# Optimization experiments

Measured on AMD Instinct MI355X. Metric: run time of the kernel, lower is better.

The kernel has to match this reference:

```python
import jax, jax.numpy as jnp
import numpy as np

N_HEADS = 18
HEAD_DIM = 16
ROPE_THETA = 10000.0
SLIDING_WINDOW = 4096


def _rotate_half(x):
    half = x.shape[-1] // 2
    return jnp.concatenate([-x[..., half:], x[..., :half]], axis=-1)


def setup_inputs() -> dict:
    key = jax.random.key(0)
    k0, k1, k2, k3, k4 = jax.random.split(key, 5)
    B, S, H = 2, 2048, 288
    std = 0.02
    return {
        "hidden_states": jax.random.normal(k0, (B, S, H), dtype=jnp.float32),
        "Wq": jax.random.normal(k1, (H, H), dtype=jnp.float32) * std,
        "Wk": jax.random.normal(k2, (H, H), dtype=jnp.float32) * std,
        "Wv": jax.random.normal(k3, (H, H), dtype=jnp.float32) * std,
        "Wo": jax.random.normal(k4, (H, H), dtype=jnp.float32) * std,
    }


def reference(hidden_states, Wq, Wk, Wv, Wo):
    B, S, H = hidden_states.shape
    nH, D = N_HEADS, HEAD_DIM

    # QKV projections (nn.Linear: y = x @ W.T), reshape to [B, nH, S, D]
    def proj(W):
        return jnp.einsum("bsh,oh->bso", hidden_states, W).reshape(B, S, nH, D).transpose(0, 2, 1, 3)

    q, k, v = proj(Wq), proj(Wk), proj(Wv)

    # Rotary embedding: position_ids = arange(S)
    pos = jnp.arange(S, dtype=jnp.float32)
    inv_freq = 1.0 / (ROPE_THETA ** (jnp.arange(0, D, 2, dtype=jnp.float32) / D))
    freqs = pos[:, None] * inv_freq[None, :]            # [S, D/2]
    emb = jnp.concatenate([freqs, freqs], axis=-1)      # [S, D]
    cos = jnp.cos(emb)[None, None, :, :]                # [1, 1, S, D]
    sin = jnp.sin(emb)[None, None, :, :]
    q = q * cos + _rotate_half(q) * sin
    k = k * cos + _rotate_half(k) * sin

    # num_key_value_groups = 1 -> repeat_kv is identity.
    scores = jnp.einsum("bhqd,bhkd->bhqk", q, k) / jnp.sqrt(jnp.float32(D))

    # Sliding-window causal mask: attend iff 0 <= i - j < window
    i = jnp.arange(S)[:, None]
    j = jnp.arange(S)[None, :]
    allowed = (j <= i) & (i - j < SLIDING_WINDOW)       # [S, S]
    neg = jnp.finfo(scores.dtype).min
    scores = jnp.where(allowed[None, None, :, :], scores, neg)

    attn = jax.nn.softmax(scores.astype(jnp.float32), axis=-1).astype(q.dtype)
    out = jnp.einsum("bhqk,bhkd->bhqd", attn, v)        # [B, nH, S, D]
    out = out.transpose(0, 2, 1, 3).reshape(B, S, H)
    return jnp.einsum("bsh,oh->bso", out, Wo)
```

## Files before the change

kernel.cpp:

```cpp
#include <hip/hip_runtime.h>
#include <hip/hip_bf16.h>
#include <math.h>

#define H_DIM 288
#define NHEADS 18
#define HEAD_D 16
#define SEQ 2048
#define BATCH 2
#define M_TOT (BATCH*SEQ)
#define XCNT (M_TOT*H_DIM)
#define WCNT (H_DIM*H_DIM)
#define NUNITS 10368
#define NQUNITS 2304

typedef _Float16 f16_t;
typedef __attribute__((ext_vector_type(2))) _Float16 half2v;
typedef __attribute__((ext_vector_type(4))) _Float16 half4v;
typedef __attribute__((ext_vector_type(8))) _Float16 half8v;
typedef __attribute__((ext_vector_type(4))) float   float4v;

__global__ __launch_bounds__(256) void cvt_f16(
    const float* __restrict__ X,
    const float* __restrict__ Wq, const float* __restrict__ Wk,
    const float* __restrict__ Wv, const float* __restrict__ Wo,
    f16_t* __restrict__ Xf, f16_t* __restrict__ Wf)
{
    int idx = blockIdx.x * 256 + threadIdx.x;
    const int X4 = XCNT/4, W4 = WCNT/4;
    if (idx >= X4 + 4*W4) return;
    const float* src; f16_t* dst; int off;
    if (idx < X4) { src = X; dst = Xf; off = idx; }
    else {
        int r = idx - X4;
        int wz = r / W4; off = r - wz*W4;
        src = (wz==0) ? Wq : (wz==1) ? Wk : (wz==2) ? Wv : Wo;
        dst = Wf + (size_t)wz*WCNT;
    }
    float4 v = ((const float4*)src)[off];
    half4v h; h[0]=(f16_t)v.x; h[1]=(f16_t)v.y; h[2]=(f16_t)v.z; h[3]=(f16_t)v.w;
    ((half4v*)dst)[off] = h;
}

__global__ __launch_bounds__(64) void qkv_mfma(
    const f16_t* __restrict__ Xf, const f16_t* __restrict__ Wf,
    f16_t* __restrict__ Q16, f16_t* __restrict__ K16, f16_t* __restrict__ Vt)
{
    const int bx = blockIdx.x;
    const int z  = bx/6;
    const int n0 = (bx - z*6)*48;
    const int m0 = blockIdx.y*32;
    const int lane = threadIdx.x & 63;
    const int n = lane & 15, quad = lane >> 4;

    const f16_t* W = Wf + (size_t)z*WCNT;

    float4v acc[2][3];
    #pragma unroll
    for (int mt = 0; mt < 2; mt++)
        #pragma unroll
        for (int nt = 0; nt < 3; nt++)
            acc[mt][nt] = (float4v){0.f,0.f,0.f,0.f};

    for (int k0 = 0; k0 < H_DIM; k0 += 32) {
        half8v a[2], b[3];
        #pragma unroll
        for (int mt = 0; mt < 2; mt++)
            a[mt] = *(const half8v*)(Xf + (size_t)(m0 + mt*16 + n)*H_DIM + k0 + quad*8);
        #pragma unroll
        for (int nt = 0; nt < 3; nt++)
            b[nt] = *(const half8v*)(W + (size_t)(n0 + nt*16 + n)*H_DIM + k0 + quad*8);
        #pragma unroll
        for (int mt = 0; mt < 2; mt++)
            #pragma unroll
            for (int nt = 0; nt < 3; nt++)
                acc[mt][nt] = __builtin_amdgcn_mfma_f32_16x16x32_f16(a[mt], b[nt], acc[mt][nt], 0, 0, 0);
    }

    if (z < 2) {
        f16_t* dst = (z == 0) ? Q16 : K16;
        const float invf_rev = exp2f(-1.6609640474436813f * (float)(n & 7))
                             * 0.15915494309189535f;
        #pragma unroll
        for (int mt = 0; mt < 2; mt++) {
            #pragma unroll
            for (int r = 0; r < 4; r++) {
                int m = m0 + mt*16 + quad*4 + r;
                int bb = m >> 11, s = m & (SEQ - 1);
                float rev = (float)s * invf_rev;
                float fr = rev - floorf(rev);
                float sn = __builtin_amdgcn_sinf(fr);
                float c  = __builtin_amdgcn_cosf(fr);
                #pragma unroll
                for (int nt = 0; nt < 3; nt++) {
                    float own = acc[mt][nt][r];
                    float par = __shfl_xor(own, 8, 64);
                    float val = (n & 8) ? fmaf(own, c, par*sn) : fmaf(own, c, -par*sn);
                    if (z == 0) val *= 0.36067376022224085f;
                    int head = (n0 >> 4) + nt;
                    dst[((size_t)((bb*NHEADS + head)*SEQ) + s)*HEAD_D + n] = (f16_t)val;
                }
            }
        }
    } else {
        #pragma unroll
        for (int mt = 0; mt < 2; mt++)
            #pragma unroll
            for (int nt = 0; nt < 3; nt++)
                #pragma unroll
                for (int r = 0; r < 4; r++) {
                    int m = m0 + mt*16 + quad*4 + r;
                    int bb = m >> 11, s = m & (SEQ - 1);
                    int head = (n0 >> 4) + nt;
                    Vt[(size_t)(bb*NHEADS + head)*(SEQ*HEAD_D)
                       + (size_t)(s >> 4)*256 + n*16 + (s & 15)] = (f16_t)acc[mt][nt][r];
                }
    }
}

__device__ __forceinline__ half4v pack4(const float p[4]) {
    half2v ab = __builtin_bit_cast(half2v, __builtin_amdgcn_cvt_pkrtz(p[0], p[1]));
    half2v cd = __builtin_bit_cast(half2v, __builtin_amdgcn_cvt_pkrtz(p[2], p[3]));
    half4v o; o[0]=ab[0]; o[1]=ab[1]; o[2]=cd[0]; o[3]=cd[1];
    return o;
}

__global__ __launch_bounds__(256) void attn_part(
    const f16_t* __restrict__ Q16, const f16_t* __restrict__ K16,
    const f16_t* __restrict__ Vt,
    float4* __restrict__ accbuf, float* __restrict__ lbuf)
{
    const int bid = blockIdx.x;
    const int swz = (bid & 7) * 324 + (bid >> 3);
    const int unit = swz*4 + (threadIdx.x >> 6);
    const int lane = threadIdx.x & 63;
    const int n = lane & 15, quad = lane >> 4;

    const int bh = unit / 288;
    const int rem = unit - bh*288;
    int g, t0;
    if      (rem < 8)   { g=0; t0=rem;     }
    else if (rem < 24)  { g=1; t0=rem-8;   }
    else if (rem < 48)  { g=2; t0=rem-24;  }
    else if (rem < 80)  { g=3; t0=rem-48;  }
    else if (rem < 120) { g=4; t0=rem-80;  }
    else if (rem < 168) { g=5; t0=rem-120; }
    else if (rem < 224) { g=6; t0=rem-168; }
    else                { g=7; t0=rem-224; }
    const int qd = t0 / (g+1);
    const int qp = 8*g + qd;
    const int chunk = t0 - qd*(g+1);
    const int q0 = qp*32;

    half4v qb0 = *(const half4v*)(Q16 + ((size_t)bh*SEQ + q0 + n)*HEAD_D + quad*4);
    half4v qb1 = *(const half4v*)(Q16 + ((size_t)bh*SEQ + q0 + 16 + n)*HEAD_D + quad*4);
    const f16_t* Kb = K16 + (size_t)bh * SEQ * HEAD_D;
    const f16_t* Vb = Vt  + (size_t)bh * SEQ * HEAD_D;
    const int loff = n*16 + quad*4;

    const float4v zero = {0.f, 0.f, 0.f, 0.f};
    float4v acc0 = zero, acc1 = zero;
    float l0 = 0.f, l1 = 0.f;

    const int lim0 = 2*qp, lim1 = 2*qp + 1;
    const int ktlo = chunk*16;
    const int kthi = min(ktlo + 15, lim1);

    if (ktlo + 15 < lim0) {
        half4v KA[16], VA[16];
        #pragma unroll
        for (int i = 0; i < 16; i++) {
            KA[i] = *(const half4v*)(Kb + (size_t)(ktlo + i)*256 + loff);
            VA[i] = *(const half4v*)(Vb + (size_t)(ktlo + i)*256 + loff);
        }
        __builtin_amdgcn_s_setprio(1);
        #pragma unroll
        for (int i = 0; i < 16; i++) {
            float4v s1 = __builtin_amdgcn_mfma_f32_16x16x16f16(KA[i], qb1, zero, 0, 0, 0);
            float4v s0 = __builtin_amdgcn_mfma_f32_16x16x16f16(KA[i], qb0, zero, 0, 0, 0);
            float p1[4], p0[4];
            #pragma unroll
            for (int r = 0; r < 4; r++) { p1[r] = __builtin_amdgcn_exp2f(s1[r]); p0[r] = __builtin_amdgcn_exp2f(s0[r]); }
            l1 += (p1[0]+p1[1]) + (p1[2]+p1[3]);
            l0 += (p0[0]+p0[1]) + (p0[2]+p0[3]);
            acc1 = __builtin_amdgcn_mfma_f32_16x16x16f16(VA[i], pack4(p1), acc1, 0, 0, 0);
            acc0 = __builtin_amdgcn_mfma_f32_16x16x16f16(VA[i], pack4(p0), acc0, 0, 0, 0);
        }
        __builtin_amdgcn_s_setprio(0);
    } else {
        int kt = ktlo;
        half4v ka = *(const half4v*)(Kb + (size_t)kt*256 + loff);
        half4v va = *(const half4v*)(Vb + (size_t)kt*256 + loff);
        for (; kt <= kthi; kt++) {
            half4v kan, van;
            if (kt < kthi) {
                kan = *(const half4v*)(Kb + (size_t)(kt+1)*256 + loff);
                van = *(const half4v*)(Vb + (size_t)(kt+1)*256 + loff);
            }
            {
                float4v s = __builtin_amdgcn_mfma_f32_16x16x16f16(ka, qb1, zero, 0, 0, 0);
                float p[4];
                #pragma unroll
                for (int r = 0; r < 4; r++) {
                    float e = __builtin_amdgcn_exp2f(s[r]);
                    p[r] = (kt == lim1 && quad*4 + r > n) ? 0.0f : e;
                }
                l1 += (p[0]+p[1]) + (p[2]+p[3]);
                acc1 = __builtin_amdgcn_mfma_f32_16x16x16f16(va, pack4(p), acc1, 0, 0, 0);
            }
            if (kt <= lim0) {
                float4v s = __builtin_amdgcn_mfma_f32_16x16x16f16(ka, qb0, zero, 0, 0, 0);
                float p[4];
                #pragma unroll
                for (int r = 0; r < 4; r++) {
                    float e = __builtin_amdgcn_exp2f(s[r]);
                    p[r] = (kt == lim0 && quad*4 + r > n) ? 0.0f : e;
                }
                l0 += (p[0]+p[1]) + (p[2]+p[3]);
                acc0 = __builtin_amdgcn_mfma_f32_16x16x16f16(va, pack4(p), acc0, 0, 0, 0);
            }
            ka = kan; va = van;
        }
    }

    float4 a0; a0.x=acc0[0]; a0.y=acc0[1]; a0.z=acc0[2]; a0.w=acc0[3];
    float4 a1; a1.x=acc1[0]; a1.y=acc1[1]; a1.z=acc1[2]; a1.w=acc1[3];
    accbuf[((size_t)unit*2 + 0)*64 + lane] = a0;
    accbuf[((size_t)unit*2 + 1)*64 + lane] = a1;
    lbuf[((size_t)unit*2 + 0)*64 + lane] = l0;
    lbuf[((size_t)unit*2 + 1)*64 + lane] = l1;
}

__global__ __launch_bounds__(256) void attn_red(
    const float4* __restrict__ accbuf, const float* __restrict__ lbuf,
    f16_t* __restrict__ Of)
{
    const int bid = blockIdx.x;
    const int swz = (bid & 7) * 72 + (bid >> 3);
    const int wid = swz*4 + (threadIdx.x >> 6);
    const int lane = threadIdx.x & 63;
    const int n = lane & 15, quad = lane >> 4;
    const int bh = wid >> 6, qp = wid & 63;
    const int b = bh / NHEADS, h = bh - b*NHEADS;
    const int g = qp >> 3, j = qp & 7;
    const int nch = g + 1;
    const int ubase = bh*288 + qp + 4*g*(g-1) + g*j;

    #pragma unroll
    for (int t = 0; t < 2; t++) {
        float4 a = {0.f, 0.f, 0.f, 0.f};
        float l = 0.f;
        #pragma unroll
        for (int c = 0; c < 8; c++) {
            const int  cc = (c < nch) ? c : (nch - 1);
            const float m = (c < nch) ? 1.0f : 0.0f;
            size_t idx = ((size_t)(ubase + cc)*2 + t)*64 + lane;
            float4 v = accbuf[idx];
            float lv = lbuf[idx];
            a.x = fmaf(v.x, m, a.x); a.y = fmaf(v.y, m, a.y);
            a.z = fmaf(v.z, m, a.z); a.w = fmaf(v.w, m, a.w);
            l   = fmaf(lv,  m, l);
        }
        l += __shfl_xor(l, 16, 64);
        l += __shfl_xor(l, 32, 64);
        float inv = 1.0f / l;
        half4v o;
        o[0]=(f16_t)(a.x*inv); o[1]=(f16_t)(a.y*inv);
        o[2]=(f16_t)(a.z*inv); o[3]=(f16_t)(a.w*inv);
        *(half4v*)(Of + (size_t)(b*SEQ + qp*32 + t*16 + n)*H_DIM + h*HEAD_D + quad*4) = o;
    }
}

__global__ __launch_bounds__(64) void out_mfma(
    const f16_t* __restrict__ Of, const f16_t* __restrict__ Wo16,
    float* __restrict__ C)
{
    const int n0 = blockIdx.x * 48;
    const int m0 = blockIdx.y * 32;
    const int lane = threadIdx.x & 63;
    const int n = lane & 15, quad = lane >> 4;

    float4v acc[2][3];
    #pragma unroll
    for (int mt = 0; mt < 2; mt++)
        #pragma unroll
        for (int nt = 0; nt < 3; nt++)
            acc[mt][nt] = (float4v){0.f,0.f,0.f,0.f};

    for (int k0 = 0; k0 < H_DIM; k0 += 32) {
        half8v a[2], b[3];
        #pragma unroll
        for (int mt = 0; mt < 2; mt++)
            a[mt] = *(const half8v*)(Of + (size_t)(m0 + mt*16 + n)*H_DIM + k0 + quad*8);
        #pragma unroll
        for (int nt = 0; nt < 3; nt++)
            b[nt] = *(const half8v*)(Wo16 + (size_t)(n0 + nt*16 + n)*H_DIM + k0 + quad*8);
        #pragma unroll
        for (int mt = 0; mt < 2; mt++)
            #pragma unroll
            for (int nt = 0; nt < 3; nt++)
                acc[mt][nt] = __builtin_amdgcn_mfma_f32_16x16x32_f16(a[mt], b[nt], acc[mt][nt], 0, 0, 0);
    }
    #pragma unroll
    for (int mt = 0; mt < 2; mt++)
        #pragma unroll
        for (int nt = 0; nt < 3; nt++)
            #pragma unroll
            for (int r = 0; r < 4; r++) {
                int m = m0 + mt*16 + quad*4 + r;
                C[(size_t)m*H_DIM + n0 + nt*16 + n] = acc[mt][nt][r];
            }
}

extern "C" void kernel_launch(void* const* d_in, const int* in_sizes, int n_in,
                              void* d_out, int out_size, void* d_ws, size_t ws_size,
                              hipStream_t stream)
{
    const float* Xh = (const float*)d_in[0];
    const float* Wq = (const float*)d_in[1];
    const float* Wk = (const float*)d_in[2];
    const float* Wv = (const float*)d_in[3];
    const float* Wo = (const float*)d_in[4];
    float* out = (float*)d_out;

    f16_t* Xf  = (f16_t*)d_ws;
    f16_t* Wf  = Xf + XCNT;
    f16_t* Q16 = Wf + 4*(size_t)WCNT;
    f16_t* K16 = Q16 + XCNT;
    f16_t* Vt  = K16 + XCNT;
    f16_t* Of  = Vt + XCNT;
    float4* accbuf = (float4*)(Of + XCNT);
    float*  lbuf   = (float*)(accbuf + (size_t)NUNITS*2*64);

    const int total4 = (XCNT + 4*WCNT)/4;
    cvt_f16<<<dim3((total4 + 255)/256), 256, 0, stream>>>(Xh, Wq, Wk, Wv, Wo, Xf, Wf);
    qkv_mfma<<<dim3(18, 128), 64, 0, stream>>>(Xf, Wf, Q16, K16, Vt);
    attn_part<<<dim3(NUNITS/4), 256, 0, stream>>>(Q16, K16, Vt, accbuf, lbuf);
    attn_red<<<dim3(NQUNITS/4), 256, 0, stream>>>(accbuf, lbuf, Of);
    out_mfma<<<dim3(6, 128), 64, 0, stream>>>(Of, Wf + 3*(size_t)WCNT, out);
}
```

Measured before the change: 113.7 us.

## Split attention and QKV work into smaller per-wave tiles for more parallelism

After: 119.6 us. +5.2%, slower.

```diff
diff --git a/kernel.cpp b/kernel.cpp
--- a/kernel.cpp
+++ b/kernel.cpp
@@ -11,6 +11,7 @@
 #define XCNT (M_TOT*H_DIM)
 #define WCNT (H_DIM*H_DIM)
 #define NUNITS 10368
+#define NUU    20736
 #define NQUNITS 2304
 
 typedef _Float16 f16_t;
@@ -48,32 +49,26 @@
     const int bx = blockIdx.x;
     const int z  = bx/6;
     const int n0 = (bx - z*6)*48;
-    const int m0 = blockIdx.y*32;
+    const int m0 = blockIdx.y*16;
     const int lane = threadIdx.x & 63;
     const int n = lane & 15, quad = lane >> 4;
 
     const f16_t* W = Wf + (size_t)z*WCNT;
 
-    float4v acc[2][3];
+    float4v acc[3];
     #pragma unroll
-    for (int mt = 0; mt < 2; mt++)
-        #pragma unroll
-        for (int nt = 0; nt < 3; nt++)
-            acc[mt][nt] = (float4v){0.f,0.f,0.f,0.f};
+    for (int nt = 0; nt < 3; nt++)
+        acc[nt] = (float4v){0.f,0.f,0.f,0.f};
 
     for (int k0 = 0; k0 < H_DIM; k0 += 32) {
-        half8v a[2], b[3];
-        #pragma unroll
-        for (int mt = 0; mt < 2; mt++)
-            a[mt] = *(const half8v*)(Xf + (size_t)(m0 + mt*16 + n)*H_DIM + k0 + quad*8);
+        half8v a = *(const half8v*)(Xf + (size_t)(m0 + n)*H_DIM + k0 + quad*8);
+        half8v b[3];
         #pragma unroll
         for (int nt = 0; nt < 3; nt++)
             b[nt] = *(const half8v*)(W + (size_t)(n0 + nt*16 + n)*H_DIM + k0 + quad*8);
         #pragma unroll
-        for (int mt = 0; mt < 2; mt++)
-            #pragma unroll
-            for (int nt = 0; nt < 3; nt++)
-                acc[mt][nt] = __builtin_amdgcn_mfma_f32_16x16x32_f16(a[mt], b[nt], acc[mt][nt], 0, 0, 0);
+        for (int nt = 0; nt < 3; nt++)
+            acc[nt] = __builtin_amdgcn_mfma_f32_16x16x32_f16(a, b[nt], acc[nt], 0, 0, 0);
     }
 
     if (z < 2) {
@@ -81,39 +76,34 @@
         const float invf_rev = exp2f(-1.6609640474436813f * (float)(n & 7))
                              * 0.15915494309189535f;
         #pragma unroll
-        for (int mt = 0; mt < 2; mt++) {
-            #pragma unroll
-            for (int r = 0; r < 4; r++) {
-                int m = m0 + mt*16 + quad*4 + r;
-                int bb = m >> 11, s = m & (SEQ - 1);
-                float rev = (float)s * invf_rev;
-                float fr = rev - floorf(rev);
-                float sn = __builtin_amdgcn_sinf(fr);
-                float c  = __builtin_amdgcn_cosf(fr);
-                #pragma unroll
-                for (int nt = 0; nt < 3; nt++) {
-                    float own = acc[mt][nt][r];
-                    float par = __shfl_xor(own, 8, 64);
-                    float val = (n & 8) ? fmaf(own, c, par*sn) : fmaf(own, c, -par*sn);
-                    if (z == 0) val *= 0.36067376022224085f;
-                    int head = (n0 >> 4) + nt;
-                    dst[((size_t)((bb*NHEADS + head)*SEQ) + s)*HEAD_D + n] = (f16_t)val;
-                }
+        for (int r = 0; r < 4; r++) {
+            int m = m0 + quad*4 + r;
+            int bb = m >> 11, s = m & (SEQ - 1);
+            float rev = (float)s * invf_rev;
+            float fr = rev - floorf(rev);
+            float sn = __builtin_amdgcn_sinf(fr);
+            float c  = __builtin_amdgcn_cosf(fr);
+            #pragma unroll
+            for (int nt = 0; nt < 3; nt++) {
+                float own = acc[nt][r];
+                float par = __shfl_xor(own, 8, 64);
+                float val = (n & 8) ? fmaf(own, c, par*sn) : fmaf(own, c, -par*sn);
+                if (z == 0) val *= 0.36067376022224085f;
+                int head = (n0 >> 4) + nt;
+                dst[((size_t)((bb*NHEADS + head)*SEQ) + s)*HEAD_D + n] = (f16_t)val;
             }
         }
     } else {
         #pragma unroll
-        for (int mt = 0; mt < 2; mt++)
-            #pragma unroll
-            for (int nt = 0; nt < 3; nt++)
-                #pragma unroll
-                for (int r = 0; r < 4; r++) {
-                    int m = m0 + mt*16 + quad*4 + r;
-                    int bb = m >> 11, s = m & (SEQ - 1);
-                    int head = (n0 >> 4) + nt;
-                    Vt[(size_t)(bb*NHEADS + head)*(SEQ*HEAD_D)
-                       + (size_t)(s >> 4)*256 + n*16 + (s & 15)] = (f16_t)acc[mt][nt][r];
-                }
+        for (int nt = 0; nt < 3; nt++)
+            #pragma unroll
+            for (int r = 0; r < 4; r++) {
+                int m = m0 + quad*4 + r;
+                int bb = m >> 11, s = m & (SEQ - 1);
+                int head = (n0 >> 4) + nt;
+                Vt[(size_t)(bb*NHEADS + head)*(SEQ*HEAD_D)
+                   + (size_t)(s >> 4)*256 + n*16 + (s & 15)] = (f16_t)acc[nt][r];
+            }
     }
 }
 
@@ -130,8 +120,9 @@
     float4* __restrict__ accbuf, float* __restrict__ lbuf)
 {
     const int bid = blockIdx.x;
-    const int swz = (bid & 7) * 324 + (bid >> 3);
-    const int unit = swz*4 + (threadIdx.x >> 6);
+    const int swz = (bid & 7) * 648 + (bid >> 3);
+    const int uu  = swz*4 + (threadIdx.x >> 6);
+    const int unit = uu >> 1, tq = uu & 1;
     const int lane = threadIdx.x & 63;
     const int n = lane & 15, quad = lane >> 4;
 
@@ -149,43 +140,42 @@
     const int qd = t0 / (g+1);
     const int qp = 8*g + qd;
     const int chunk = t0 - qd*(g+1);
-    const int q0 = qp*32;
-
-    half4v qb0 = *(const half4v*)(Q16 + ((size_t)bh*SEQ + q0 + n)*HEAD_D + quad*4);
-    half4v qb1 = *(const half4v*)(Q16 + ((size_t)bh*SEQ + q0 + 16 + n)*HEAD_D + quad*4);
+
+    half4v qb = *(const half4v*)(Q16 + ((size_t)bh*SEQ + qp*32 + tq*16 + n)*HEAD_D + quad*4);
     const f16_t* Kb = K16 + (size_t)bh * SEQ * HEAD_D;
     const f16_t* Vb = Vt  + (size_t)bh * SEQ * HEAD_D;
     const int loff = n*16 + quad*4;
 
     const float4v zero = {0.f, 0.f, 0.f, 0.f};
-    float4v acc0 = zero, acc1 = zero;
-    float l0 = 0.f, l1 = 0.f;
-
-    const int lim0 = 2*qp, lim1 = 2*qp + 1;
+    float4v acc = zero;
+    float l = 0.f;
+
+    const int lim  = 2*qp + tq;
     const int ktlo = chunk*16;
-    const int kthi = min(ktlo + 15, lim1);
-
-    if (ktlo + 15 < lim0) {
-        half4v KA[16], VA[16];
-        #pragma unroll
-        for (int i = 0; i < 16; i++) {
-            KA[i] = *(const half4v*)(Kb + (size_t)(ktlo + i)*256 + loff);
-            VA[i] = *(const half4v*)(Vb + (size_t)(ktlo + i)*256 + loff);
+    const int kthi = min(ktlo + 15, lim);
+
+    if (ktlo + 15 < lim) {
+        #pragma unroll 1
+        for (int hb = 0; hb < 2; hb++) {
+            const int kb = ktlo + hb*8;
+            half4v KA[8], VA[8];
+            #pragma unroll
+            for (int i = 0; i < 8; i++) {
+                KA[i] = *(const half4v*)(Kb + (size_t)(kb + i)*256 + loff);
+                VA[i] = *(const half4v*)(Vb + (size_t)(kb + i)*256 + loff);
+            }
+            __builtin_amdgcn_s_setprio(1);
+            #pragma unroll
+            for (int i = 0; i < 8; i++) {
+                float4v s = __builtin_amdgcn_mfma_f32_16x16x16f16(KA[i], qb, zero, 0, 0, 0);
+                float p[4];
+                #pragma unroll
+                for (int r = 0; r < 4; r++) p[r] = __builtin_amdgcn_exp2f(s[r]);
+                l += (p[0]+p[1]) + (p[2]+p[3]);
+                acc = __builtin_amdgcn_mfma_f32_16x16x16f16(VA[i], pack4(p), acc, 0, 0, 0);
+            }
+            __builtin_amdgcn_s_setprio(0);
         }
-        __builtin_amdgcn_s_setprio(1);
-        #pragma unroll
-        for (int i = 0; i < 16; i++) {
-            float4v s1 = __builtin_amdgcn_mfma_f32_16x16x16f16(KA[i], qb1, zero, 0, 0, 0);
-            float4v s0 = __builtin_amdgcn_mfma_f32_16x16x16f16(KA[i], qb0, zero, 0, 0, 0);
-            float p1[4], p0[4];
-            #pragma unroll
-            for (int r = 0; r < 4; r++) { p1[r] = __builtin_amdgcn_exp2f(s1[r]); p0[r] = __builtin_amdgcn_exp2f(s0[r]); }
-            l1 += (p1[0]+p1[1]) + (p1[2]+p1[3]);
-            l0 += (p0[0]+p0[1]) + (p0[2]+p0[3]);
-            acc1 = __builtin_amdgcn_mfma_f32_16x16x16f16(VA[i], pack4(p1), acc1, 0, 0, 0);
-            acc0 = __builtin_amdgcn_mfma_f32_16x16x16f16(VA[i], pack4(p0), acc0, 0, 0, 0);
-        }
-        __builtin_amdgcn_s_setprio(0);
     } else {
         int kt = ktlo;
         half4v ka = *(const half4v*)(Kb + (size_t)kt*256 + loff);
@@ -196,38 +186,22 @@
                 kan = *(const half4v*)(Kb + (size_t)(kt+1)*256 + loff);
                 van = *(const half4v*)(Vb + (size_t)(kt+1)*256 + loff);
             }
-            {
-                float4v s = __builtin_amdgcn_mfma_f32_16x16x16f16(ka, qb1, zero, 0, 0, 0);
-                float p[4];
-                #pragma unroll
-                for (int r = 0; r < 4; r++) {
-                    float e = __builtin_amdgcn_exp2f(s[r]);
-                    p[r] = (kt == lim1 && quad*4 + r > n) ? 0.0f : e;
-                }
-                l1 += (p[0]+p[1]) + (p[2]+p[3]);
-                acc1 = __builtin_amdgcn_mfma_f32_16x16x16f16(va, pack4(p), acc1, 0, 0, 0);
-            }
-            if (kt <= lim0) {
-                float4v s = __builtin_amdgcn_mfma_f32_16x16x16f16(ka, qb0, zero, 0, 0, 0);
-                float p[4];
-                #pragma unroll
-                for (int r = 0; r < 4; r++) {
-                    float e = __builtin_amdgcn_exp2f(s[r]);
-                    p[r] = (kt == lim0 && quad*4 + r > n) ? 0.0f : e;
-                }
-                l0 += (p[0]+p[1]) + (p[2]+p[3]);
-                acc0 = __builtin_amdgcn_mfma_f32_16x16x16f16(va, pack4(p), acc0, 0, 0, 0);
-            }
+            float4v s = __builtin_amdgcn_mfma_f32_16x16x16f16(ka, qb, zero, 0, 0, 0);
+            float p[4];
+            #pragma unroll
+            for (int r = 0; r < 4; r++) {
+                float e = __builtin_amdgcn_exp2f(s[r]);
+                p[r] = (kt == lim && quad*4 + r > n) ? 0.0f : e;
+            }
+            l += (p[0]+p[1]) + (p[2]+p[3]);
+            acc = __builtin_amdgcn_mfma_f32_16x16x16f16(va, pack4(p), acc, 0, 0, 0);
             ka = kan; va = van;
         }
     }
 
-    float4 a0; a0.x=acc0[0]; a0.y=acc0[1]; a0.z=acc0[2]; a0.w=acc0[3];
-    float4 a1; a1.x=acc1[0]; a1.y=acc1[1]; a1.z=acc1[2]; a1.w=acc1[3];
-    accbuf[((size_t)unit*2 + 0)*64 + lane] = a0;
-    accbuf[((size_t)unit*2 + 1)*64 + lane] = a1;
-    lbuf[((size_t)unit*2 + 0)*64 + lane] = l0;
-    lbuf[((size_t)unit*2 + 1)*64 + lane] = l1;
+    float4 a0; a0.x=acc[0]; a0.y=acc[1]; a0.z=acc[2]; a0.w=acc[3];
+    accbuf[((size_t)unit*2 + tq)*64 + lane] = a0;
+    lbuf  [((size_t)unit*2 + tq)*64 + lane] = l;
 }
 
 __global__ __launch_bounds__(256) void attn_red(
@@ -333,8 +307,8 @@
 
     const int total4 = (XCNT + 4*WCNT)/4;
     cvt_f16<<<dim3((total4 + 255)/256), 256, 0, stream>>>(Xh, Wq, Wk, Wv, Wo, Xf, Wf);
-    qkv_mfma<<<dim3(18, 128), 64, 0, stream>>>(Xf, Wf, Q16, K16, Vt);
-    attn_part<<<dim3(NUNITS/4), 256, 0, stream>>>(Q16, K16, Vt, accbuf, lbuf);
+    qkv_mfma<<<dim3(18, 256), 64, 0, stream>>>(Xf, Wf, Q16, K16, Vt);
+    attn_part<<<dim3(NUU/4), 256, 0, stream>>>(Q16, K16, Vt, accbuf, lbuf);
     attn_red<<<dim3(NQUNITS/4), 256, 0, stream>>>(accbuf, lbuf, Of);
     out_mfma<<<dim3(6, 128), 64, 0, stream>>>(Of, Wf + 3*(size_t)WCNT, out);
 }
```
